# Kernel tuning notes

Measured on AMD Instinct MI355X. Metric: run time of the kernel, lower is better.

Reference implementation:

```python
import jax, jax.numpy as jnp
import numpy as np

B, T = 32, 64
I, O, H = 64, 64, 512
N, W = 128, 64           # memory slots, slot width
IF = 3 * W + 6           # interface size


def setup_inputs() -> dict:
    key = jax.random.key(0)
    ks = jax.random.split(key, 6)
    s = 0.05
    return {
        "x": jax.random.normal(ks[0], (B, T, I), jnp.float32),
        "W_ih": jax.random.normal(ks[1], (4 * H, I + W), jnp.float32) * s,
        "W_hh": jax.random.normal(ks[2], (4 * H, H), jnp.float32) * s,
        "b_ih": jnp.zeros((4 * H,), jnp.float32),
        "b_hh": jnp.zeros((4 * H,), jnp.float32),
        "W_if": jax.random.normal(ks[3], (IF, H), jnp.float32) * s,
        "b_if": jnp.zeros((IF,), jnp.float32),
        "W_out": jax.random.normal(ks[4], (O, H + W), jnp.float32) * s,
        "b_out": jnp.zeros((O,), jnp.float32),
    }


def reference(x, W_ih, W_hh, b_ih, b_hh, W_if, b_if, W_out, b_out):
    Bb, Tt, _ = x.shape
    dt = x.dtype
    eye = jnp.eye(N, dtype=dt)
    batch_idx = jnp.arange(Bb)[:, None]

    def step(carry, x_t):
        h, c, mem, usage, prec, link, rw, rvec = carry
        # --- LSTM controller (PyTorch gate order i,f,g,o) ---
        inp = jnp.concatenate([x_t, rvec], axis=-1)
        gates = inp @ W_ih.T + h @ W_hh.T + b_ih + b_hh
        i_g, f_g, g_g, o_g = jnp.split(gates, 4, axis=-1)
        c = jax.nn.sigmoid(f_g) * c + jax.nn.sigmoid(i_g) * jnp.tanh(g_g)
        h = jax.nn.sigmoid(o_g) * jnp.tanh(c)
        itf = h @ W_if.T + b_if
        # --- parse interface ---
        erase = jax.nn.sigmoid(itf[:, :W])
        wvec = itf[:, W:2 * W]
        wg = jax.nn.sigmoid(itf[:, 2 * W])
        ag = jax.nn.sigmoid(itf[:, 2 * W + 1])
        rstr = jnp.log1p(jnp.exp(itf[:, 3 * W + 2]))  # softplus
        # --- allocation weighting (sort usage asc, shifted cumprod, scatter) ---
        idx = jnp.argsort(usage, axis=-1)
        usage_sorted = jnp.take_along_axis(usage, idx, axis=-1)
        cprod = jnp.cumprod(usage_sorted, axis=-1)
        cprod = jnp.concatenate([jnp.ones((Bb, 1), dt), cprod[:, :-1]], axis=-1)
        alloc_in_order = (1.0 - usage_sorted) * cprod
        alloc = jnp.zeros_like(usage).at[batch_idx, idx].set(alloc_in_order)
        ww = wg[:, None] * ag[:, None] * alloc  # [B,N]
        # --- erase + add write ---
        mem = mem * (1.0 - ww[:, :, None] * erase[:, None, :]) + ww[:, :, None] * wvec[:, None, :]
        usage = usage + (1.0 - usage) * ww
        # --- temporal link / precedence ---
        ww_ij = ww[:, :, None] + ww[:, None, :]
        link = (1.0 - ww_ij) * link + prec[:, :, None] * ww[:, None, :]
        link = link * (1.0 - eye)
        prec = (1.0 - ww.sum(-1, keepdims=True)) * prec + ww
        # --- read weights (NOTE: source uses itf[:, :W] as read key) ---
        rmode = jax.nn.softmax(itf[:, -3:], axis=-1)
        rkey = itf[:, :W]
        dot = jnp.einsum('bw,bnw->bn', rkey, mem)
        kn = jnp.linalg.norm(rkey, axis=-1, keepdims=True) + 1e-8
        mn = jnp.linalg.norm(mem, axis=-1) + 1e-8
        cw = jax.nn.softmax(dot / (kn * mn) * rstr[:, None], axis=-1)
        bw = jnp.einsum('bnm,bn->bm', link, rw)   # link^T @ rw
        fw = jnp.einsum('bnm,bm->bn', link, rw)   # link @ rw
        wts = rmode[:, 0:1] * bw + rmode[:, 1:2] * fw + rmode[:, 2:3] * cw + 1e-8
        wts = wts / wts.sum(-1, keepdims=True)
        rvec = jnp.einsum('bn,bnw->bw', wts, mem)
        out = jnp.concatenate([h, rvec], axis=-1) @ W_out.T + b_out
        return (h, c, mem, usage, prec, link, wts, rvec), out

    z = lambda *s: jnp.zeros(s, dt)
    carry0 = (z(Bb, H), z(Bb, H), z(Bb, N, W), z(Bb, N), z(Bb, N), z(Bb, N, N), z(Bb, N), z(Bb, W))
    _, outs = jax.lax.scan(step, carry0, jnp.swapaxes(x, 0, 1))
    return jnp.swapaxes(outs, 0, 1)  # [B,T,O]
```

## Files before the change

kernel.cpp:

```cpp
#include <hip/hip_runtime.h>
#include <math.h>

#define Bb 32
#define Tt 64
#define Ii 64
#define Oo 64
#define Hh 512
#define Nn 128
#define Wd 64
#define IFs 198
#define KV 640
#define G4 2048

#define NP1 128
#define NWG 160
#define NT 512

#define P2_MEM    0
#define P2_H      8320
#define P2_SCR    8896
#define P2_ITF    10944
#define P2_ERASE  11168
#define P2_WVEC   11232
#define P2_USAGE  11296
#define P2_PREC   11424
#define P2_RW     11552
#define P2_WW     11680
#define P2_SCAN   11808
#define P2_SS     11936
#define P2_SCAL   12064
#define P2_BIF    12080
#define P2_ALLOC  12304
#define P1_WIF    0
#define P1_BS     13464
#define P1_V      13720
#define P1_CC     15016
#define P1_HSL    15144
#define P1_PACC   15272
#define SMEM_FLOATS 23592
#define SMEM_BYTES (SMEM_FLOATS * 4)

#define S_WWSUM 0

__device__ __align__(16) float g_WT[KV * G4];
__device__ __align__(16) float g_bsum[G4];
typedef unsigned long long u64;
__device__ u64 g_h64[2 * Bb * Hh];
__device__ u64 g_rv64[Bb * Wd];
__device__ u64 g_if64[Bb * 8 * 200];

__device__ __forceinline__ float sigf(float v) { return 1.f / (1.f + expf(-v)); }

__device__ __forceinline__ u64 ldrelax(const u64* p) {
  return __hip_atomic_load(p, __ATOMIC_RELAXED, __HIP_MEMORY_SCOPE_AGENT);
}
__device__ __forceinline__ void tstore(u64* p, unsigned tag, float v) {
  u64 val = ((u64)tag << 32) | (u64)__float_as_uint(v);
  __hip_atomic_store(p, val, __ATOMIC_RELAXED, __HIP_MEMORY_SCOPE_AGENT);
}
__device__ __forceinline__ float tval(u64 v) {
  return __uint_as_float((unsigned)(v & 0xffffffffu));
}
__device__ __forceinline__ void waitpair(const u64* p0, const u64* p1,
                                         u64& v0, u64& v1, unsigned tag) {
  while (((unsigned)(v0 >> 32)) != tag || ((unsigned)(v1 >> 32)) != tag) {
    __builtin_amdgcn_s_sleep(1);
    v0 = ldrelax(p0);
    v1 = ldrelax(p1);
  }
}
__device__ __forceinline__ void waitquad(const u64* p0, const u64* p1,
                                         const u64* p2, const u64* p3,
                                         u64& v0, u64& v1, u64& v2, u64& v3,
                                         unsigned tag) {
  while (((unsigned)(v0 >> 32)) != tag || ((unsigned)(v1 >> 32)) != tag ||
         ((unsigned)(v2 >> 32)) != tag || ((unsigned)(v3 >> 32)) != tag) {
    __builtin_amdgcn_s_sleep(1);
    v0 = ldrelax(p0);
    v1 = ldrelax(p1);
    v2 = ldrelax(p2);
    v3 = ldrelax(p3);
  }
}

#define TIN 512
__global__ __launch_bounds__(TIN) void dnc_init(const float* __restrict__ W_ih,
                                                const float* __restrict__ W_hh,
                                                const float* __restrict__ b_ih,
                                                const float* __restrict__ b_hh) {
  __shared__ float tile[64][65];
  const int tid = threadIdx.x;
  int i0 = blockIdx.x * blockDim.x + tid;
  int st = gridDim.x * blockDim.x;
  for (int idx = i0; idx < G4; idx += st) g_bsum[idx] = b_ih[idx] + b_hh[idx];
  for (int idx = i0; idx < 2 * Bb * Hh; idx += st) g_h64[idx] = 0ull;
  for (int idx = i0; idx < Bb * Wd; idx += st) g_rv64[idx] = 0ull;
  for (int idx = i0; idx < Bb * 8 * 200; idx += st) g_if64[idx] = 0ull;

  for (int tileId = blockIdx.x; tileId < 320; tileId += gridDim.x) {
    int tc = tileId >> 5, tj = tileId & 31;
    for (int k = tid; k < 64 * 64; k += TIN) {
      int r = k >> 6, cl = k & 63;
      int j = tj * 64 + r, c = tc * 64 + cl;
      tile[r][cl] = (c < 128) ? W_ih[j * 128 + c] : W_hh[j * 512 + (c - 128)];
    }
    __syncthreads();
    for (int k = tid; k < 64 * 64; k += TIN) {
      int cl = k >> 6, rjj = k & 63;
      int c = tc * 64 + cl;
      int rp = (c < 128) ? (512 + c) : (c - 128);
      g_WT[(size_t)rp * G4 + tj * 64 + rjj] = tile[rjj][cl];
    }
    __syncthreads();
  }
}

__global__ __launch_bounds__(NT) void dnc_main(const float* __restrict__ x,
                                               const float* __restrict__ W_if,
                                               const float* __restrict__ b_if,
                                               const float* __restrict__ W_out,
                                               const float* __restrict__ b_out,
                                               float* __restrict__ out) {
  extern __shared__ float sm[];
  const int tid = threadIdx.x;
  const int wg = blockIdx.x;

  if (wg < NP1) {
    const int jb = wg & 7;
    const int bb = wg >> 3;
    const int b0 = bb * 2;
    for (int i = tid; i < IFs * 64; i += NT) {
      int o = i >> 6, c = i & 63;
      sm[P1_WIF + o * 68 + c] = W_if[(size_t)o * Hh + jb * 64 + c];
    }
    if (tid < 64) {
      int gq = tid >> 4, m = tid & 15;
      ((float4*)(sm + P1_BS))[tid] = ((const float4*)g_bsum)[gq * 128 + jb * 16 + m];
    }
    if (tid < 128) sm[P1_CC + tid] = 0.f;
    __syncthreads();

    for (int t = 0; t < Tt; ++t) {
      {
        const u64* hsrc = g_h64 + (size_t)((t + 1) & 1) * (Bb * Hh);
        const int u = tid;
        const u64* a0 = hsrc + (size_t)b0 * Hh + u;
        const u64* a1 = hsrc + (size_t)(b0 + 1) * Hh + u;
        u64 v0 = ldrelax(a0), v1 = ldrelax(a1);
        waitpair(a0, a1, v0, v1, (unsigned)t);
        float2 hh;
        hh.x = tval(v0);
        hh.y = tval(v1);
        *(float2*)(sm + P1_V + u * 2) = hh;
        if (tid < 128) {
          const int bl2 = tid >> 6, i = tid & 63;
          float xv = x[((size_t)(b0 + bl2) * Tt + t) * Ii + i];
          sm[P1_V + (512 + i) * 2 + bl2] = xv;
        }
      }
      __syncthreads();

      {
        const int fg = tid & 31, ks = tid >> 5;
        const int fcolA = ((fg >> 4) * 128) + jb * 16 + (fg & 15);
        const float* v2 = sm + P1_V + ks * 80;
        const float4* wpA = (const float4*)g_WT + (size_t)(ks * 40) * 512 + fcolA;
        if (ks >= 14) {
          const int j = tid & 63;
          const u64* r0 = g_rv64 + (size_t)b0 * Wd + j;
          const u64* r1 = g_rv64 + (size_t)(b0 + 1) * Wd + j;
          u64 u0 = ldrelax(r0), u1 = ldrelax(r1);
          waitpair(r0, r1, u0, u1, (unsigned)t);
          float2 rv;
          rv.x = tval(u0);
          rv.y = tval(u1);
          *(float2*)(sm + P1_V + (576 + j) * 2) = rv;
        }
        float4 aA0 = {0.f, 0.f, 0.f, 0.f}, aA1 = {0.f, 0.f, 0.f, 0.f};
        float4 aB0 = {0.f, 0.f, 0.f, 0.f}, aB1 = {0.f, 0.f, 0.f, 0.f};
#pragma unroll 4
        for (int r = 0; r < 40; ++r) {
          float4 wA = wpA[(size_t)r * 512];
          float4 wB = wpA[(size_t)r * 512 + 256];
          float2 vv = *(const float2*)(v2 + r * 2);
          aA0.x += wA.x * vv.x; aA0.y += wA.y * vv.x; aA0.z += wA.z * vv.x; aA0.w += wA.w * vv.x;
          aA1.x += wA.x * vv.y; aA1.y += wA.y * vv.y; aA1.z += wA.z * vv.y; aA1.w += wA.w * vv.y;
          aB0.x += wB.x * vv.x; aB0.y += wB.y * vv.x; aB0.z += wB.z * vv.x; aB0.w += wB.w * vv.x;
          aB1.x += wB.x * vv.y; aB1.y += wB.y * vv.y; aB1.z += wB.z * vv.y; aB1.w += wB.w * vv.y;
        }
        float4* pacc = (float4*)(sm + P1_PACC);
        pacc[(ks * 2 + 0) * 65 + fg] = aA0;
        pacc[(ks * 2 + 1) * 65 + fg] = aA1;
        pacc[(ks * 2 + 0) * 65 + fg + 32] = aB0;
        pacc[(ks * 2 + 1) * 65 + fg + 32] = aB1;
      }
      __syncthreads();
      if (tid < 128) {
        const int bl = tid >> 6, l = tid & 63;
        const float* pb = sm + P1_PACC + bl * 260 + l;
        float gv0 = 0.f, gv1 = 0.f, gv2 = 0.f, gv3 = 0.f;
#pragma unroll
        for (int ks = 0; ks < 16; ++ks) {
          const float* pk = pb + ks * 520;
          gv0 += pk[0];
          gv1 += pk[64];
          gv2 += pk[128];
          gv3 += pk[192];
        }
        float ig = gv0 + sm[P1_BS + l];
        float fg = gv1 + sm[P1_BS + 64 + l];
        float gg = gv2 + sm[P1_BS + 128 + l];
        float og = gv3 + sm[P1_BS + 192 + l];
        float co = sm[P1_CC + bl * 64 + l];
        float cn = sigf(fg) * co + sigf(ig) * tanhf(gg);
        float hn = sigf(og) * tanhf(cn);
        sm[P1_CC + bl * 64 + l] = cn;
        sm[P1_HSL + bl * 64 + l] = hn;
        tstore(g_h64 + (size_t)(t & 1) * (Bb * Hh) + (size_t)(b0 + bl) * Hh + jb * 64 + l,
               (unsigned)(t + 1), hn);
      }
      __syncthreads();
      if (tid < 2 * IFs) {
        const int o = tid >> 1, bl = tid & 1;
        const float4* wr = (const float4*)(sm + P1_WIF + o * 68);
        const float4* h4 = (const float4*)(sm + P1_HSL + bl * 64);
        float acc = 0.f;
#pragma unroll 8
        for (int c4 = 0; c4 < 16; ++c4) {
          float4 w = wr[c4]; float4 h = h4[c4];
          acc += w.x * h.x + w.y * h.y + w.z * h.z + w.w * h.w;
        }
        tstore(g_if64 + ((size_t)(b0 + bl) * 8 + jb) * 200 + o, (unsigned)(t + 1), acc);
      }
    }
  } else {
    const int b = wg - NP1;
    float* SCR = sm + P2_SCR;
    float regL[32], regLT[32];
#pragma unroll
    for (int k = 0; k < 32; ++k) { regL[k] = 0.f; regLT[k] = 0.f; }
    for (int i = tid; i < Nn * 65; i += NT) sm[P2_MEM + i] = 0.f;
    if (tid < 128) { sm[P2_USAGE + tid] = 0.f; sm[P2_PREC + tid] = 0.f; sm[P2_RW + tid] = 0.f; }
    if (tid < IFs) sm[P2_BIF + tid] = b_if[tid];
    __syncthreads();
    if (tid < 64) {
      const int li = tid, i0 = 2 * li, i1 = i0 + 1;
      float u0 = sm[P2_USAGE + i0], u1 = sm[P2_USAGE + i1];
      int r0 = 0, r1 = 0;
      for (int jc = 0; jc < 32; ++jc) {
        float4 uj4 = *(const float4*)(sm + P2_USAGE + jc * 4);
#pragma unroll
        for (int e = 0; e < 4; ++e) {
          float uj = (&uj4.x)[e];
          int j = jc * 4 + e;
          r0 += (uj < u0 || (uj == u0 && j < i0)) ? 1 : 0;
          r1 += (uj < u1 || (uj == u1 && j < i1)) ? 1 : 0;
        }
      }
      sm[P2_SS + r0] = u0;
      sm[P2_SS + r1] = u1;
      float s0 = sm[P2_SS + i0], s1 = sm[P2_SS + i1];
      float p = s0 * s1;
#pragma unroll
      for (int off = 1; off < 64; off <<= 1) {
        float v = __shfl_up(p, off, 64);
        if (li >= off) p *= v;
      }
      float E = __shfl_up(p, 1, 64);
      if (li == 0) E = 1.f;
      sm[P2_SCAN + i0] = E * s0;
      sm[P2_SCAN + i1] = E * s0 * s1;
      float ex0 = (r0 > 0) ? sm[P2_SCAN + r0 - 1] : 1.f;
      float ex1 = (r1 > 0) ? sm[P2_SCAN + r1 - 1] : 1.f;
      sm[P2_ALLOC + i0] = (1.f - u0) * ex0;
      sm[P2_ALLOC + i1] = (1.f - u1) * ex1;
    }
    __syncthreads();

    for (int t = 0; t < Tt; ++t) {
      if (tid < 2 * IFs) {
        const int o = tid >> 1, hf = tid & 1;
        const u64* src = g_if64 + ((size_t)b * 8 + hf * 4) * 200 + o;
        u64 a0 = ldrelax(src), a1 = ldrelax(src + 200),
            a2 = ldrelax(src + 400), a3 = ldrelax(src + 600);
        waitquad(src, src + 200, src + 400, src + 600, a0, a1, a2, a3,
                 (unsigned)(t + 1));
        float s = tval(a0) + tval(a1) + tval(a2) + tval(a3);
        s += __shfl_xor(s, 1, 64);
        if (hf == 0) sm[P2_ITF + o] = s + sm[P2_BIF + o];
      }
      __syncthreads();
      float kn_r = 0.f, rstr_r = 0.f, rm0_r = 0.f, rm1_r = 0.f, rm2_r = 0.f;
      if (tid < 64) {
        const int li = tid, i0 = 2 * li, i1 = i0 + 1;
        float wgag = sigf(sm[P2_ITF + 128]) * sigf(sm[P2_ITF + 129]);
        float rs = sm[P2_ITF + 194];
        rstr_r = (rs > 20.f) ? rs : log1pf(expf(rs));
        float m0 = sm[P2_ITF + 195], m1 = sm[P2_ITF + 196], m2 = sm[P2_ITF + 197];
        float mx = fmaxf(m0, fmaxf(m1, m2));
        float e0 = expf(m0 - mx), e1 = expf(m1 - mx), e2 = expf(m2 - mx);
        float es = e0 + e1 + e2;
        rm0_r = e0 / es; rm1_r = e1 / es; rm2_r = e2 / es;
        float rk = sm[P2_ITF + li];
        sm[P2_ERASE + li] = sigf(rk);
        sm[P2_WVEC + li] = sm[P2_ITF + 64 + li];
        float sq = rk * rk;
#pragma unroll
        for (int off = 32; off > 0; off >>= 1) sq += __shfl_xor(sq, off, 64);
        kn_r = sqrtf(sq) + 1e-8f;
        float u0 = sm[P2_USAGE + i0], u1 = sm[P2_USAGE + i1];
        float w0 = wgag * sm[P2_ALLOC + i0];
        float w1 = wgag * sm[P2_ALLOC + i1];
        sm[P2_WW + i0] = w0; sm[P2_WW + i1] = w1;
        sm[P2_USAGE + i0] = u0 + (1.f - u0) * w0;
        sm[P2_USAGE + i1] = u1 + (1.f - u1) * w1;
        float wws = w0 + w1;
#pragma unroll
        for (int off = 32; off > 0; off >>= 1) wws += __shfl_xor(wws, off, 64);
        if (li == 0) sm[P2_SCAL + S_WWSUM] = wws;
      }
      __syncthreads();
      {
        const int n = tid & 127, ws = tid >> 7;
        float4 er[4], wv[4], kf[4];
#pragma unroll
        for (int r = 0; r < 4; ++r) {
          er[r] = *(const float4*)(sm + P2_ERASE + ws * 16 + r * 4);
          wv[r] = *(const float4*)(sm + P2_WVEC + ws * 16 + r * 4);
          kf[r] = *(const float4*)(sm + P2_ITF + ws * 16 + r * 4);
        }
        float wwn = sm[P2_WW + n];
        float dotp = 0.f, mnp = 0.f;
        const int base = P2_MEM + n * 65 + ws * 16;
#pragma unroll
        for (int q = 0; q < 16; ++q) {
          float m = sm[base + q];
          float ee = (&er[q >> 2].x)[q & 3];
          float vv = (&wv[q >> 2].x)[q & 3];
          float kk = (&kf[q >> 2].x)[q & 3];
          m = m * (1.f - wwn * ee) + wwn * vv;
          sm[base + q] = m;
          dotp += kk * m;
          mnp += m * m;
        }
        SCR[ws * 128 + n] = dotp;
        SCR[512 + ws * 128 + n] = mnp;
        const int m = n, ns = ws;
        float wwm = wwn;
        float prn = sm[P2_PREC + m];
        float bwp = 0.f, fwp = 0.f;
#pragma unroll
        for (int kq = 0; kq < 8; ++kq) {
          float4 ww4 = *(const float4*)(sm + P2_WW + ns * 32 + kq * 4);
          float4 pr4 = *(const float4*)(sm + P2_PREC + ns * 32 + kq * 4);
          float4 rw4 = *(const float4*)(sm + P2_RW + ns * 32 + kq * 4);
#pragma unroll
          for (int e = 0; e < 4; ++e) {
            int k = kq * 4 + e;
            int nn = ns * 32 + k;
            float wwo = (&ww4.x)[e];
            float pro = (&pr4.x)[e];
            float rwo = (&rw4.x)[e];
            float L = regL[k];
            L = (1.f - wwo - wwm) * L + pro * wwm;
            if (nn == m) L = 0.f;
            regL[k] = L;
            bwp += L * rwo;
            float LT = regLT[k];
            LT = (1.f - wwm - wwo) * LT + prn * wwo;
            if (nn == m) LT = 0.f;
            regLT[k] = LT;
            fwp += LT * rwo;
          }
        }
        SCR[1024 + ns * 128 + m] = bwp;
        SCR[1536 + ns * 128 + m] = fwp;
      }
      __syncthreads();
      if (tid < 64) {
        int i0 = 2 * tid, i1 = i0 + 1;
        float d0 = SCR[i0] + SCR[128 + i0] + SCR[256 + i0] + SCR[384 + i0];
        float d1 = SCR[i1] + SCR[128 + i1] + SCR[256 + i1] + SCR[384 + i1];
        float mn0 = sqrtf(SCR[512 + i0] + SCR[640 + i0] + SCR[768 + i0] + SCR[896 + i0]) + 1e-8f;
        float mn1 = sqrtf(SCR[512 + i1] + SCR[640 + i1] + SCR[768 + i1] + SCR[896 + i1]) + 1e-8f;
        float bw0 = SCR[1024 + i0] + SCR[1152 + i0] + SCR[1280 + i0] + SCR[1408 + i0];
        float bw1 = SCR[1024 + i1] + SCR[1152 + i1] + SCR[1280 + i1] + SCR[1408 + i1];
        float fw0 = SCR[1536 + i0] + SCR[1664 + i0] + SCR[1792 + i0] + SCR[1920 + i0];
        float fw1 = SCR[1536 + i1] + SCR[1664 + i1] + SCR[1792 + i1] + SCR[1920 + i1];
        float q0 = d0 / (kn_r * mn0) * rstr_r;
        float q1 = d1 / (kn_r * mn1) * rstr_r;
        float mx = fmaxf(q0, q1);
#pragma unroll
        for (int off = 32; off > 0; off >>= 1) mx = fmaxf(mx, __shfl_xor(mx, off, 64));
        float e0 = expf(q0 - mx), e1 = expf(q1 - mx);
        float es = e0 + e1;
#pragma unroll
        for (int off = 32; off > 0; off >>= 1) es += __shfl_xor(es, off, 64);
        float wv0 = rm0_r * bw0 + rm1_r * fw0 + rm2_r * (e0 / es) + 1e-8f;
        float wv1 = rm0_r * bw1 + rm1_r * fw1 + rm2_r * (e1 / es) + 1e-8f;
        float wsum = wv0 + wv1;
#pragma unroll
        for (int off = 32; off > 0; off >>= 1) wsum += __shfl_xor(wsum, off, 64);
        sm[P2_RW + i0] = wv0 / wsum;
        sm[P2_RW + i1] = wv1 / wsum;
      }
      __syncthreads();
      {
        const int w = tid & 63, ns8 = tid >> 6;
        float4 rw4[4];
#pragma unroll
        for (int r = 0; r < 4; ++r)
          rw4[r] = *(const float4*)(sm + P2_RW + ns8 * 16 + r * 4);
        float p = 0.f;
#pragma unroll
        for (int k = 0; k < 16; ++k)
          p += (&rw4[k >> 2].x)[k & 3] * sm[P2_MEM + (ns8 * 16 + k) * 65 + w];
        SCR[ns8 * 64 + w] = p;
      }
      __syncthreads();
      if (tid < 64) {
        float r = 0.f;
#pragma unroll
        for (int s2 = 0; s2 < 8; ++s2) r += SCR[s2 * 64 + tid];
        sm[P2_H + 512 + tid] = r;
        tstore(g_rv64 + (size_t)b * Wd + tid, (unsigned)(t + 1), r);
      } else if (tid < 320) {
        const int idx = tid - 64;
        const u64* hsrc = g_h64 + (size_t)(t & 1) * (Bb * Hh) + (size_t)b * Hh;
        const u64* a0 = hsrc + idx * 2;
        const u64* a1 = hsrc + idx * 2 + 1;
        u64 v0 = ldrelax(a0), v1 = ldrelax(a1);
        waitpair(a0, a1, v0, v1, (unsigned)(t + 1));
        sm[P2_H + idx * 2] = tval(v0);
        sm[P2_H + idx * 2 + 1] = tval(v1);
      } else if (tid < 384) {
        const int li = tid - 320, i0 = 2 * li, i1 = i0 + 1;
        float u0 = sm[P2_USAGE + i0], u1 = sm[P2_USAGE + i1];
        int r0 = 0, r1 = 0;
        for (int jc = 0; jc < 32; ++jc) {
          float4 uj4 = *(const float4*)(sm + P2_USAGE + jc * 4);
#pragma unroll
          for (int e = 0; e < 4; ++e) {
            float uj = (&uj4.x)[e];
            int j = jc * 4 + e;
            r0 += (uj < u0 || (uj == u0 && j < i0)) ? 1 : 0;
            r1 += (uj < u1 || (uj == u1 && j < i1)) ? 1 : 0;
          }
        }
        sm[P2_SS + r0] = u0;
        sm[P2_SS + r1] = u1;
        float s0 = sm[P2_SS + i0], s1 = sm[P2_SS + i1];
        float p = s0 * s1;
#pragma unroll
        for (int off = 1; off < 64; off <<= 1) {
          float v = __shfl_up(p, off, 64);
          if (li >= off) p *= v;
        }
        float E = __shfl_up(p, 1, 64);
        if (li == 0) E = 1.f;
        sm[P2_SCAN + i0] = E * s0;
        sm[P2_SCAN + i1] = E * s0 * s1;
        float ex0 = (r0 > 0) ? sm[P2_SCAN + r0 - 1] : 1.f;
        float ex1 = (r1 > 0) ? sm[P2_SCAN + r1 - 1] : 1.f;
        sm[P2_ALLOC + i0] = (1.f - u0) * ex0;
        sm[P2_ALLOC + i1] = (1.f - u1) * ex1;
      } else {
        const int n = tid - 384;
        float wws = sm[P2_SCAL + S_WWSUM];
        sm[P2_PREC + n] = (1.f - wws) * sm[P2_PREC + n] + sm[P2_WW + n];
      }
      __syncthreads();
      {
        const int o = tid >> 3, seg = tid & 7;
        const float4* wrow = (const float4*)(W_out + (size_t)o * 576) + seg * 18;
        const float4* hb = (const float4*)(sm + P2_H) + seg * 18;
        float p = 0.f;
#pragma unroll
        for (int q = 0; q < 18; ++q) {
          float4 w = wrow[q]; float4 h = hb[q];
          p += w.x * h.x + w.y * h.y + w.z * h.z + w.w * h.w;
        }
        p += __shfl_down(p, 4, 8);
        p += __shfl_down(p, 2, 8);
        p += __shfl_down(p, 1, 8);
        if (seg == 0) out[((size_t)b * Tt + t) * Oo + o] = p + b_out[o];
      }
    }
  }
}

extern "C" void kernel_launch(void* const* d_in, const int* in_sizes, int n_in,
                              void* d_out, int out_size, void* d_ws, size_t ws_size,
                              hipStream_t stream) {
  (void)in_sizes; (void)n_in; (void)d_ws; (void)ws_size; (void)out_size;
  const float* x    = (const float*)d_in[0];
  const float* W_ih = (const float*)d_in[1];
  const float* W_hh = (const float*)d_in[2];
  const float* b_ih = (const float*)d_in[3];
  const float* b_hh = (const float*)d_in[4];
  const float* W_if = (const float*)d_in[5];
  const float* b_if = (const float*)d_in[6];
  const float* W_out = (const float*)d_in[7];
  const float* b_out = (const float*)d_in[8];
  float* out = (float*)d_out;

  dnc_init<<<320, TIN, 0, stream>>>(W_ih, W_hh, b_ih, b_hh);

  hipFuncSetAttribute((const void*)dnc_main,
                      hipFuncAttributeMaxDynamicSharedMemorySize, SMEM_BYTES);

  void* args[] = {(void*)&x, (void*)&W_if, (void*)&b_if,
                  (void*)&W_out, (void*)&b_out, (void*)&out};
  hipLaunchCooperativeKernel((void*)dnc_main, dim3(NWG), dim3(NT), args,
                             SMEM_BYTES, stream);
}
```

Baseline: 866.0 us.

## Retile LSTM phase to four batches by 32 hidden units per workgroup

The controller workgroups switch from covering 2 batch rows by 64 hidden units to 4 batch rows by 32 hidden units. Each weight float4 loaded from global memory is now reused across four batch rows instead of two, which halves per-workgroup weight traffic in the gate GEMV. The cost is that each workgroup waits on four batch rows of h and rvec per step. The memory-phase workgroups must also poll and sum 16 interface partials instead of 8, so cross-workgroup synchronization traffic goes up.

```diff
diff --git a/kernel.cpp b/kernel.cpp
--- a/kernel.cpp
+++ b/kernel.cpp
@@ -32,11 +32,11 @@
 #define P2_BIF    12080
 #define P2_ALLOC  12304
 #define P1_WIF    0
-#define P1_BS     13464
-#define P1_V      13720
-#define P1_CC     15016
-#define P1_HSL    15144
-#define P1_PACC   15272
+#define P1_BS     7128
+#define P1_V      7256
+#define P1_CC     9816
+#define P1_HSL    9944
+#define P1_PACC   10072
 #define SMEM_FLOATS 23592
 #define SMEM_BYTES (SMEM_FLOATS * 4)
 
@@ -47,7 +47,7 @@
 typedef unsigned long long u64;
 __device__ u64 g_h64[2 * Bb * Hh];
 __device__ u64 g_rv64[Bb * Wd];
-__device__ u64 g_if64[Bb * 8 * 200];
+__device__ u64 g_if64[Bb * 16 * 200];
 
 __device__ __forceinline__ float sigf(float v) { return 1.f / (1.f + expf(-v)); }
 
@@ -95,7 +95,7 @@
   for (int idx = i0; idx < G4; idx += st) g_bsum[idx] = b_ih[idx] + b_hh[idx];
   for (int idx = i0; idx < 2 * Bb * Hh; idx += st) g_h64[idx] = 0ull;
   for (int idx = i0; idx < Bb * Wd; idx += st) g_rv64[idx] = 0ull;
-  for (int idx = i0; idx < Bb * 8 * 200; idx += st) g_if64[idx] = 0ull;
+  for (int idx = i0; idx < Bb * 16 * 200; idx += st) g_if64[idx] = 0ull;
 
   for (int tileId = blockIdx.x; tileId < 320; tileId += gridDim.x) {
     int tc = tileId >> 5, tj = tileId & 31;
@@ -126,111 +126,118 @@
   const int wg = blockIdx.x;
 
   if (wg < NP1) {
-    const int jb = wg & 7;
-    const int bb = wg >> 3;
-    const int b0 = bb * 2;
-    for (int i = tid; i < IFs * 64; i += NT) {
-      int o = i >> 6, c = i & 63;
-      sm[P1_WIF + o * 68 + c] = W_if[(size_t)o * Hh + jb * 64 + c];
-    }
-    if (tid < 64) {
-      int gq = tid >> 4, m = tid & 15;
-      ((float4*)(sm + P1_BS))[tid] = ((const float4*)g_bsum)[gq * 128 + jb * 16 + m];
-    }
-    if (tid < 128) sm[P1_CC + tid] = 0.f;
+    const int jb = wg >> 3;
+    const int bb = wg & 7;
+    const int b0 = bb * 4;
+    for (int i = tid; i < IFs * 32; i += NT) {
+      int o = i >> 5, c = i & 31;
+      sm[P1_WIF + o * 36 + c] = W_if[(size_t)o * Hh + jb * 32 + c];
+    }
+    if (tid < 128) {
+      int g = tid >> 5, l = tid & 31;
+      sm[P1_BS + tid] = g_bsum[g * 512 + jb * 32 + l];
+      sm[P1_CC + tid] = 0.f;
+    }
     __syncthreads();
 
     for (int t = 0; t < Tt; ++t) {
       {
         const u64* hsrc = g_h64 + (size_t)((t + 1) & 1) * (Bb * Hh);
         const int u = tid;
-        const u64* a0 = hsrc + (size_t)b0 * Hh + u;
+        const u64* a0 = hsrc + (size_t)(b0 + 0) * Hh + u;
         const u64* a1 = hsrc + (size_t)(b0 + 1) * Hh + u;
-        u64 v0 = ldrelax(a0), v1 = ldrelax(a1);
-        waitpair(a0, a1, v0, v1, (unsigned)t);
-        float2 hh;
-        hh.x = tval(v0);
-        hh.y = tval(v1);
-        *(float2*)(sm + P1_V + u * 2) = hh;
-        if (tid < 128) {
+        const u64* a2 = hsrc + (size_t)(b0 + 2) * Hh + u;
+        const u64* a3 = hsrc + (size_t)(b0 + 3) * Hh + u;
+        u64 v0 = ldrelax(a0), v1 = ldrelax(a1), v2 = ldrelax(a2), v3 = ldrelax(a3);
+        waitquad(a0, a1, a2, a3, v0, v1, v2, v3, (unsigned)t);
+        float4 hh;
+        hh.x = tval(v0); hh.y = tval(v1); hh.z = tval(v2); hh.w = tval(v3);
+        ((float4*)(sm + P1_V))[u] = hh;
+        if (tid < 256) {
           const int bl2 = tid >> 6, i = tid & 63;
-          float xv = x[((size_t)(b0 + bl2) * Tt + t) * Ii + i];
-          sm[P1_V + (512 + i) * 2 + bl2] = xv;
+          sm[P1_V + (512 + i) * 4 + bl2] = x[((size_t)(b0 + bl2) * Tt + t) * Ii + i];
         }
       }
       __syncthreads();
 
       {
         const int fg = tid & 31, ks = tid >> 5;
-        const int fcolA = ((fg >> 4) * 128) + jb * 16 + (fg & 15);
-        const float* v2 = sm + P1_V + ks * 80;
-        const float4* wpA = (const float4*)g_WT + (size_t)(ks * 40) * 512 + fcolA;
+        const int fcol = ((fg >> 3) * 128) + jb * 8 + (fg & 7);
+        const float4* vp = (const float4*)(sm + P1_V) + ks * 40;
+        const float4* wp = (const float4*)g_WT + (size_t)(ks * 40) * 512 + fcol;
         if (ks >= 14) {
           const int j = tid & 63;
-          const u64* r0 = g_rv64 + (size_t)b0 * Wd + j;
+          const u64* r0 = g_rv64 + (size_t)(b0 + 0) * Wd + j;
           const u64* r1 = g_rv64 + (size_t)(b0 + 1) * Wd + j;
-          u64 u0 = ldrelax(r0), u1 = ldrelax(r1);
-          waitpair(r0, r1, u0, u1, (unsigned)t);
-          float2 rv;
-          rv.x = tval(u0);
-          rv.y = tval(u1);
-          *(float2*)(sm + P1_V + (576 + j) * 2) = rv;
-        }
-        float4 aA0 = {0.f, 0.f, 0.f, 0.f}, aA1 = {0.f, 0.f, 0.f, 0.f};
-        float4 aB0 = {0.f, 0.f, 0.f, 0.f}, aB1 = {0.f, 0.f, 0.f, 0.f};
+          const u64* r2 = g_rv64 + (size_t)(b0 + 2) * Wd + j;
+          const u64* r3 = g_rv64 + (size_t)(b0 + 3) * Wd + j;
+          u64 u0 = ldrelax(r0), u1 = ldrelax(r1), u2 = ldrelax(r2), u3 = ldrelax(r3);
+          waitquad(r0, r1, r2, r3, u0, u1, u2, u3, (unsigned)t);
+          float4 rv;
+          rv.x = tval(u0); rv.y = tval(u1); rv.z = tval(u2); rv.w = tval(u3);
+          ((float4*)(sm + P1_V))[576 + j] = rv;
+        }
+        float4 a0 = {0.f, 0.f, 0.f, 0.f}, a1 = {0.f, 0.f, 0.f, 0.f};
+        float4 a2 = {0.f, 0.f, 0.f, 0.f}, a3 = {0.f, 0.f, 0.f, 0.f};
 #pragma unroll 4
         for (int r = 0; r < 40; ++r) {
-          float4 wA = wpA[(size_t)r * 512];
-          float4 wB = wpA[(size_t)r * 512 + 256];
-          float2 vv = *(const float2*)(v2 + r * 2);
-          aA0.x += wA.x * vv.x; aA0.y += wA.y * vv.x; aA0.z += wA.z * vv.x; aA0.w += wA.w * vv.x;
-          aA1.x += wA.x * vv.y; aA1.y += wA.y * vv.y; aA1.z += wA.z * vv.y; aA1.w += wA.w * vv.y;
-          aB0.x += wB.x * vv.x; aB0.y += wB.y * vv.x; aB0.z += wB.z * vv.x; aB0.w += wB.w * vv.x;
-          aB1.x += wB.x * vv.y; aB1.y += wB.y * vv.y; aB1.z += wB.z * vv.y; aB1.w += wB.w * vv.y;
+          float4 w4 = wp[(size_t)r * 512];
+          float4 vv = vp[r];
+          a0.x += w4.x * vv.x; a0.y += w4.y * vv.x; a0.z += w4.z * vv.x; a0.w += w4.w * vv.x;
+          a1.x += w4.x * vv.y; a1.y += w4.y * vv.y; a1.z += w4.z * vv.y; a1.w += w4.w * vv.y;
+          a2.x += w4.x * vv.z; a2.y += w4.y * vv.z; a2.z += w4.z * vv.z; a2.w += w4.w * vv.z;
+          a3.x += w4.x * vv.w; a3.y += w4.y * vv.w; a3.z += w4.z * vv.w; a3.w += w4.w * vv.w;
         }
         float4* pacc = (float4*)(sm + P1_PACC);
-        pacc[(ks * 2 + 0) * 65 + fg] = aA0;
-        pacc[(ks * 2 + 1) * 65 + fg] = aA1;
-        pacc[(ks * 2 + 0) * 65 + fg + 32] = aB0;
-        pacc[(ks * 2 + 1) * 65 + fg + 32] = aB1;
+        pacc[(ks * 4 + 0) * 33 + fg] = a0;
+        pacc[(ks * 4 + 1) * 33 + fg] = a1;
+        pacc[(ks * 4 + 2) * 33 + fg] = a2;
+        pacc[(ks * 4 + 3) * 33 + fg] = a3;
       }
       __syncthreads();
       if (tid < 128) {
-        const int bl = tid >> 6, l = tid & 63;
-        const float* pb = sm + P1_PACC + bl * 260 + l;
+        const int bl = tid >> 5, l = tid & 31;
+        const float* pb = sm + P1_PACC + bl * 132 + l;
         float gv0 = 0.f, gv1 = 0.f, gv2 = 0.f, gv3 = 0.f;
 #pragma unroll
         for (int ks = 0; ks < 16; ++ks) {
-          const float* pk = pb + ks * 520;
+          const float* pk = pb + ks * 528;
           gv0 += pk[0];
-          gv1 += pk[64];
-          gv2 += pk[128];
-          gv3 += pk[192];
+          gv1 += pk[32];
+          gv2 += pk[64];
+          gv3 += pk[96];
         }
         float ig = gv0 + sm[P1_BS + l];
-        float fg = gv1 + sm[P1_BS + 64 + l];
-        float gg = gv2 + sm[P1_BS + 128 + l];
-        float og = gv3 + sm[P1_BS + 192 + l];
-        float co = sm[P1_CC + bl * 64 + l];
+        float fg = gv1 + sm[P1_BS + 32 + l];
+        float gg = gv2 + sm[P1_BS + 64 + l];
+        float og = gv3 + sm[P1_BS + 96 + l];
+        float co = sm[P1_CC + tid];
         float cn = sigf(fg) * co + sigf(ig) * tanhf(gg);
         float hn = sigf(og) * tanhf(cn);
-        sm[P1_CC + bl * 64 + l] = cn;
-        sm[P1_HSL + bl * 64 + l] = hn;
-        tstore(g_h64 + (size_t)(t & 1) * (Bb * Hh) + (size_t)(b0 + bl) * Hh + jb * 64 + l,
+        sm[P1_CC + tid] = cn;
+        sm[P1_HSL + tid] = hn;
+        tstore(g_h64 + (size_t)(t & 1) * (Bb * Hh) + (size_t)(b0 + bl) * Hh + jb * 32 + l,
                (unsigned)(t + 1), hn);
       }
       __syncthreads();
       if (tid < 2 * IFs) {
-        const int o = tid >> 1, bl = tid & 1;
-        const float4* wr = (const float4*)(sm + P1_WIF + o * 68);
-        const float4* h4 = (const float4*)(sm + P1_HSL + bl * 64);
-        float acc = 0.f;
-#pragma unroll 8
-        for (int c4 = 0; c4 < 16; ++c4) {
-          float4 w = wr[c4]; float4 h = h4[c4];
-          acc += w.x * h.x + w.y * h.y + w.z * h.z + w.w * h.w;
-        }
-        tstore(g_if64 + ((size_t)(b0 + bl) * 8 + jb) * 200 + o, (unsigned)(t + 1), acc);
+        const int o = tid >> 1, blh = tid & 1;
+        const float4* wr = (const float4*)(sm + P1_WIF + o * 36);
+        const float4* hA = (const float4*)(sm + P1_HSL) + (blh * 2 + 0) * 8;
+        const float4* hB = (const float4*)(sm + P1_HSL) + (blh * 2 + 1) * 8;
+        float accA = 0.f, accB = 0.f;
+#pragma unroll
+        for (int c4 = 0; c4 < 8; ++c4) {
+          float4 w = wr[c4];
+          float4 ha = hA[c4];
+          float4 hb = hB[c4];
+          accA += w.x * ha.x + w.y * ha.y + w.z * ha.z + w.w * ha.w;
+          accB += w.x * hb.x + w.y * hb.y + w.z * hb.z + w.w * hb.w;
+        }
+        tstore(g_if64 + ((size_t)(b0 + blh * 2 + 0) * 16 + jb) * 200 + o,
+               (unsigned)(t + 1), accA);
+        tstore(g_if64 + ((size_t)(b0 + blh * 2 + 1) * 16 + jb) * 200 + o,
+               (unsigned)(t + 1), accB);
       }
     }
   } else {
@@ -280,12 +287,22 @@
     for (int t = 0; t < Tt; ++t) {
       if (tid < 2 * IFs) {
         const int o = tid >> 1, hf = tid & 1;
-        const u64* src = g_if64 + ((size_t)b * 8 + hf * 4) * 200 + o;
-        u64 a0 = ldrelax(src), a1 = ldrelax(src + 200),
-            a2 = ldrelax(src + 400), a3 = ldrelax(src + 600);
-        waitquad(src, src + 200, src + 400, src + 600, a0, a1, a2, a3,
-                 (unsigned)(t + 1));
-        float s = tval(a0) + tval(a1) + tval(a2) + tval(a3);
+        const u64* base = g_if64 + ((size_t)b * 16 + hf * 8) * 200 + o;
+        const u64 *q0 = base, *q1 = base + 200, *q2 = base + 400, *q3 = base + 600;
+        const u64 *q4 = base + 800, *q5 = base + 1000, *q6 = base + 1200, *q7 = base + 1400;
+        u64 w0 = ldrelax(q0), w1 = ldrelax(q1), w2 = ldrelax(q2), w3 = ldrelax(q3);
+        u64 w4 = ldrelax(q4), w5 = ldrelax(q5), w6 = ldrelax(q6), w7 = ldrelax(q7);
+        const unsigned tg = (unsigned)(t + 1);
+        while (((unsigned)(w0 >> 32)) != tg || ((unsigned)(w1 >> 32)) != tg ||
+               ((unsigned)(w2 >> 32)) != tg || ((unsigned)(w3 >> 32)) != tg ||
+               ((unsigned)(w4 >> 32)) != tg || ((unsigned)(w5 >> 32)) != tg ||
+               ((unsigned)(w6 >> 32)) != tg || ((unsigned)(w7 >> 32)) != tg) {
+          __builtin_amdgcn_s_sleep(1);
+          w0 = ldrelax(q0); w1 = ldrelax(q1); w2 = ldrelax(q2); w3 = ldrelax(q3);
+          w4 = ldrelax(q4); w5 = ldrelax(q5); w6 = ldrelax(q6); w7 = ldrelax(q7);
+        }
+        float s = tval(w0) + tval(w1) + tval(w2) + tval(w3)
+                + tval(w4) + tval(w5) + tval(w6) + tval(w7);
         s += __shfl_xor(s, 1, 64);
         if (hf == 0) sm[P2_ITF + o] = s + sm[P2_BIF + o];
       }
```

After: 987.5 us. +14.0%, slower.

## Compute only live interface rows and fold write-weight prep into later phases

Applied to the files above, without the earlier changes.

The interface projection now computes only the 134 rows that are actually consumed (key/erase, write vector, gates, read strength, read modes), skipping the unused middle rows, which shrinks the per-step W_if dot products and the cross-workgroup polling traffic. The separate write-weight/usage phase and its barrier are removed. Instead the allocation weights are double-buffered with a precomputed sum, so ww is derived inline as wgag*alloc, and the usage update moves into the sort phase. Read-mode and key-norm work moves into the read-weight phase. This drops one block-wide synchronisation per timestep, at the cost of recomputing a few sigmoids in several threads.

```diff
diff --git a/kernel.cpp b/kernel.cpp
--- a/kernel.cpp
+++ b/kernel.cpp
@@ -9,6 +9,7 @@
 #define Nn 128
 #define Wd 64
 #define IFs 198
+#define LIVE 134
 #define KV 640
 #define G4 2048
 
@@ -21,11 +22,9 @@
 #define P2_SCR    8896
 #define P2_ITF    10944
 #define P2_ERASE  11168
-#define P2_WVEC   11232
 #define P2_USAGE  11296
 #define P2_PREC   11424
 #define P2_RW     11552
-#define P2_WW     11680
 #define P2_SCAN   11808
 #define P2_SS     11936
 #define P2_SCAL   12064
@@ -40,8 +39,6 @@
 #define SMEM_FLOATS 23592
 #define SMEM_BYTES (SMEM_FLOATS * 4)
 
-#define S_WWSUM 0
-
 __device__ __align__(16) float g_WT[KV * G4];
 __device__ __align__(16) float g_bsum[G4];
 typedef unsigned long long u64;
@@ -129,9 +126,10 @@
     const int jb = wg & 7;
     const int bb = wg >> 3;
     const int b0 = bb * 2;
-    for (int i = tid; i < IFs * 64; i += NT) {
-      int o = i >> 6, c = i & 63;
-      sm[P1_WIF + o * 68 + c] = W_if[(size_t)o * Hh + jb * 64 + c];
+    for (int i = tid; i < LIVE * 64; i += NT) {
+      int slot = i >> 6, c = i & 63;
+      int oo = (slot < 130) ? slot : slot + 64;
+      sm[P1_WIF + slot * 68 + c] = W_if[(size_t)oo * Hh + jb * 64 + c];
     }
     if (tid < 64) {
       int gq = tid >> 4, m = tid & 15;
@@ -220,9 +218,9 @@
                (unsigned)(t + 1), hn);
       }
       __syncthreads();
-      if (tid < 2 * IFs) {
-        const int o = tid >> 1, bl = tid & 1;
-        const float4* wr = (const float4*)(sm + P1_WIF + o * 68);
+      if (tid < 2 * LIVE) {
+        const int slot = tid >> 1, bl = tid & 1;
+        const float4* wr = (const float4*)(sm + P1_WIF + slot * 68);
         const float4* h4 = (const float4*)(sm + P1_HSL + bl * 64);
         float acc = 0.f;
 #pragma unroll 8
@@ -230,7 +228,7 @@
           float4 w = wr[c4]; float4 h = h4[c4];
           acc += w.x * h.x + w.y * h.y + w.z * h.z + w.w * h.w;
         }
-        tstore(g_if64 + ((size_t)(b0 + bl) * 8 + jb) * 200 + o, (unsigned)(t + 1), acc);
+        tstore(g_if64 + ((size_t)(b0 + bl) * 8 + jb) * 200 + slot, (unsigned)(t + 1), acc);
       }
     }
   } else {
@@ -241,7 +239,7 @@
     for (int k = 0; k < 32; ++k) { regL[k] = 0.f; regLT[k] = 0.f; }
     for (int i = tid; i < Nn * 65; i += NT) sm[P2_MEM + i] = 0.f;
     if (tid < 128) { sm[P2_USAGE + tid] = 0.f; sm[P2_PREC + tid] = 0.f; sm[P2_RW + tid] = 0.f; }
-    if (tid < IFs) sm[P2_BIF + tid] = b_if[tid];
+    if (tid < LIVE) sm[P2_BIF + tid] = b_if[(tid < 130) ? tid : tid + 64];
     __syncthreads();
     if (tid < 64) {
       const int li = tid, i0 = 2 * li, i1 = i0 + 1;
@@ -272,64 +270,47 @@
       sm[P2_SCAN + i1] = E * s0 * s1;
       float ex0 = (r0 > 0) ? sm[P2_SCAN + r0 - 1] : 1.f;
       float ex1 = (r1 > 0) ? sm[P2_SCAN + r1 - 1] : 1.f;
-      sm[P2_ALLOC + i0] = (1.f - u0) * ex0;
-      sm[P2_ALLOC + i1] = (1.f - u1) * ex1;
+      float a0 = (1.f - u0) * ex0;
+      float a1 = (1.f - u1) * ex1;
+      sm[P2_ALLOC + i0] = a0;
+      sm[P2_ALLOC + i1] = a1;
+      float as = a0 + a1;
+#pragma unroll
+      for (int off = 32; off > 0; off >>= 1) as += __shfl_xor(as, off, 64);
+      if (li == 0) sm[P2_SCAL + 0] = as;
     }
     __syncthreads();
 
     for (int t = 0; t < Tt; ++t) {
-      if (tid < 2 * IFs) {
-        const int o = tid >> 1, hf = tid & 1;
-        const u64* src = g_if64 + ((size_t)b * 8 + hf * 4) * 200 + o;
+      if (tid < 2 * LIVE) {
+        const int slot = tid >> 1, hf = tid & 1;
+        const u64* src = g_if64 + ((size_t)b * 8 + hf * 4) * 200 + slot;
         u64 a0 = ldrelax(src), a1 = ldrelax(src + 200),
             a2 = ldrelax(src + 400), a3 = ldrelax(src + 600);
         waitquad(src, src + 200, src + 400, src + 600, a0, a1, a2, a3,
                  (unsigned)(t + 1));
         float s = tval(a0) + tval(a1) + tval(a2) + tval(a3);
         s += __shfl_xor(s, 1, 64);
-        if (hf == 0) sm[P2_ITF + o] = s + sm[P2_BIF + o];
-      }
-      __syncthreads();
-      float kn_r = 0.f, rstr_r = 0.f, rm0_r = 0.f, rm1_r = 0.f, rm2_r = 0.f;
-      if (tid < 64) {
-        const int li = tid, i0 = 2 * li, i1 = i0 + 1;
-        float wgag = sigf(sm[P2_ITF + 128]) * sigf(sm[P2_ITF + 129]);
-        float rs = sm[P2_ITF + 194];
-        rstr_r = (rs > 20.f) ? rs : log1pf(expf(rs));
-        float m0 = sm[P2_ITF + 195], m1 = sm[P2_ITF + 196], m2 = sm[P2_ITF + 197];
-        float mx = fmaxf(m0, fmaxf(m1, m2));
-        float e0 = expf(m0 - mx), e1 = expf(m1 - mx), e2 = expf(m2 - mx);
-        float es = e0 + e1 + e2;
-        rm0_r = e0 / es; rm1_r = e1 / es; rm2_r = e2 / es;
-        float rk = sm[P2_ITF + li];
-        sm[P2_ERASE + li] = sigf(rk);
-        sm[P2_WVEC + li] = sm[P2_ITF + 64 + li];
-        float sq = rk * rk;
-#pragma unroll
-        for (int off = 32; off > 0; off >>= 1) sq += __shfl_xor(sq, off, 64);
-        kn_r = sqrtf(sq) + 1e-8f;
-        float u0 = sm[P2_USAGE + i0], u1 = sm[P2_USAGE + i1];
-        float w0 = wgag * sm[P2_ALLOC + i0];
-        float w1 = wgag * sm[P2_ALLOC + i1];
-        sm[P2_WW + i0] = w0; sm[P2_WW + i1] = w1;
-        sm[P2_USAGE + i0] = u0 + (1.f - u0) * w0;
-        sm[P2_USAGE + i1] = u1 + (1.f - u1) * w1;
-        float wws = w0 + w1;
-#pragma unroll
-        for (int off = 32; off > 0; off >>= 1) wws += __shfl_xor(wws, off, 64);
-        if (li == 0) sm[P2_SCAL + S_WWSUM] = wws;
+        if (hf == 0) {
+          float v = s + sm[P2_BIF + slot];
+          int oo = (slot < 130) ? slot : slot + 64;
+          sm[P2_ITF + oo] = v;
+          if (oo < 64) sm[P2_ERASE + oo] = sigf(v);
+        }
       }
       __syncthreads();
       {
         const int n = tid & 127, ws = tid >> 7;
+        const float* ALo = sm + P2_ALLOC + (t & 1) * 128;
+        const float wgag = sigf(sm[P2_ITF + 128]) * sigf(sm[P2_ITF + 129]);
         float4 er[4], wv[4], kf[4];
 #pragma unroll
         for (int r = 0; r < 4; ++r) {
           er[r] = *(const float4*)(sm + P2_ERASE + ws * 16 + r * 4);
-          wv[r] = *(const float4*)(sm + P2_WVEC + ws * 16 + r * 4);
+          wv[r] = *(const float4*)(sm + P2_ITF + 64 + ws * 16 + r * 4);
           kf[r] = *(const float4*)(sm + P2_ITF + ws * 16 + r * 4);
         }
-        float wwn = sm[P2_WW + n];
+        float wwn = wgag * ALo[n];
         float dotp = 0.f, mnp = 0.f;
         const int base = P2_MEM + n * 65 + ws * 16;
 #pragma unroll
@@ -351,14 +332,14 @@
         float bwp = 0.f, fwp = 0.f;
 #pragma unroll
         for (int kq = 0; kq < 8; ++kq) {
-          float4 ww4 = *(const float4*)(sm + P2_WW + ns * 32 + kq * 4);
+          float4 al4 = *(const float4*)(ALo + ns * 32 + kq * 4);
           float4 pr4 = *(const float4*)(sm + P2_PREC + ns * 32 + kq * 4);
           float4 rw4 = *(const float4*)(sm + P2_RW + ns * 32 + kq * 4);
 #pragma unroll
           for (int e = 0; e < 4; ++e) {
             int k = kq * 4 + e;
             int nn = ns * 32 + k;
-            float wwo = (&ww4.x)[e];
+            float wwo = wgag * (&al4.x)[e];
             float pro = (&pr4.x)[e];
             float rwo = (&rw4.x)[e];
             float L = regL[k];
@@ -378,7 +359,22 @@
       }
       __syncthreads();
       if (tid < 64) {
-        int i0 = 2 * tid, i1 = i0 + 1;
+        const int li = tid;
+        float rs = sm[P2_ITF + 194];
+        float rstr = (rs > 20.f) ? rs : log1pf(expf(rs));
+        float m0 = sm[P2_ITF + 195], m1 = sm[P2_ITF + 196], m2 = sm[P2_ITF + 197];
+        float mxm = fmaxf(m0, fmaxf(m1, m2));
+        float e0m = expf(m0 - mxm), e1m = expf(m1 - mxm), e2m = expf(m2 - mxm);
+        float esm = e0m + e1m + e2m;
+        float rm0 = e0m / esm, rm1 = e1m / esm, rm2 = e2m / esm;
+        float sq = 0.f;
+#pragma unroll
+        for (int c4 = 0; c4 < 16; ++c4) {
+          float4 k4 = *(const float4*)(sm + P2_ITF + c4 * 4);
+          sq += k4.x * k4.x + k4.y * k4.y + k4.z * k4.z + k4.w * k4.w;
+        }
+        float kn = sqrtf(sq) + 1e-8f;
+        int i0 = 2 * li, i1 = i0 + 1;
         float d0 = SCR[i0] + SCR[128 + i0] + SCR[256 + i0] + SCR[384 + i0];
         float d1 = SCR[i1] + SCR[128 + i1] + SCR[256 + i1] + SCR[384 + i1];
         float mn0 = sqrtf(SCR[512 + i0] + SCR[640 + i0] + SCR[768 + i0] + SCR[896 + i0]) + 1e-8f;
@@ -387,8 +383,8 @@
         float bw1 = SCR[1024 + i1] + SCR[1152 + i1] + SCR[1280 + i1] + SCR[1408 + i1];
         float fw0 = SCR[1536 + i0] + SCR[1664 + i0] + SCR[1792 + i0] + SCR[1920 + i0];
         float fw1 = SCR[1536 + i1] + SCR[1664 + i1] + SCR[1792 + i1] + SCR[1920 + i1];
-        float q0 = d0 / (kn_r * mn0) * rstr_r;
-        float q1 = d1 / (kn_r * mn1) * rstr_r;
+        float q0 = d0 / (kn * mn0) * rstr;
+        float q1 = d1 / (kn * mn1) * rstr;
         float mx = fmaxf(q0, q1);
 #pragma unroll
         for (int off = 32; off > 0; off >>= 1) mx = fmaxf(mx, __shfl_xor(mx, off, 64));
@@ -396,8 +392,8 @@
         float es = e0 + e1;
 #pragma unroll
         for (int off = 32; off > 0; off >>= 1) es += __shfl_xor(es, off, 64);
-        float wv0 = rm0_r * bw0 + rm1_r * fw0 + rm2_r * (e0 / es) + 1e-8f;
-        float wv1 = rm0_r * bw1 + rm1_r * fw1 + rm2_r * (e1 / es) + 1e-8f;
+        float wv0 = rm0 * bw0 + rm1 * fw0 + rm2 * (e0 / es) + 1e-8f;
+        float wv1 = rm0 * bw1 + rm1 * fw1 + rm2 * (e1 / es) + 1e-8f;
         float wsum = wv0 + wv1;
 #pragma unroll
         for (int off = 32; off > 0; off >>= 1) wsum += __shfl_xor(wsum, off, 64);
@@ -435,7 +431,13 @@
         sm[P2_H + idx * 2 + 1] = tval(v1);
       } else if (tid < 384) {
         const int li = tid - 320, i0 = 2 * li, i1 = i0 + 1;
-        float u0 = sm[P2_USAGE + i0], u1 = sm[P2_USAGE + i1];
+        const float* ALo = sm + P2_ALLOC + (t & 1) * 128;
+        float wgag = sigf(sm[P2_ITF + 128]) * sigf(sm[P2_ITF + 129]);
+        float u0o = sm[P2_USAGE + i0], u1o = sm[P2_USAGE + i1];
+        float u0 = u0o + (1.f - u0o) * (wgag * ALo[i0]);
+        float u1 = u1o + (1.f - u1o) * (wgag * ALo[i1]);
+        sm[P2_USAGE + i0] = u0;
+        sm[P2_USAGE + i1] = u1;
         int r0 = 0, r1 = 0;
         for (int jc = 0; jc < 32; ++jc) {
           float4 uj4 = *(const float4*)(sm + P2_USAGE + jc * 4);
@@ -462,12 +464,21 @@
         sm[P2_SCAN + i1] = E * s0 * s1;
         float ex0 = (r0 > 0) ? sm[P2_SCAN + r0 - 1] : 1.f;
         float ex1 = (r1 > 0) ? sm[P2_SCAN + r1 - 1] : 1.f;
-        sm[P2_ALLOC + i0] = (1.f - u0) * ex0;
-        sm[P2_ALLOC + i1] = (1.f - u1) * ex1;
+        float a0 = (1.f - u0) * ex0;
+        float a1 = (1.f - u1) * ex1;
+        float* ALn = sm + P2_ALLOC + ((t + 1) & 1) * 128;
+        ALn[i0] = a0;
+        ALn[i1] = a1;
+        float as = a0 + a1;
+#pragma unroll
+        for (int off = 32; off > 0; off >>= 1) as += __shfl_xor(as, off, 64);
+        if (li == 0) sm[P2_SCAL + ((t + 1) & 1)] = as;
       } else {
         const int n = tid - 384;
-        float wws = sm[P2_SCAL + S_WWSUM];
-        sm[P2_PREC + n] = (1.f - wws) * sm[P2_PREC + n] + sm[P2_WW + n];
+        float wgag = sigf(sm[P2_ITF + 128]) * sigf(sm[P2_ITF + 129]);
+        float wws = wgag * sm[P2_SCAL + (t & 1)];
+        sm[P2_PREC + n] = (1.f - wws) * sm[P2_PREC + n]
+                        + wgag * sm[P2_ALLOC + (t & 1) * 128 + n];
       }
       __syncthreads();
       {
```

Result: slower. 913.1 us (+5.4%).
